# Optimization experiments

Hardware: AMD Instinct MI355X
Metric: run time of the kernel (lower is better)

The kernel has to match this reference:

```python
import jax, jax.numpy as jnp
import numpy as np

N = 10000
E = 320000
C = 16


def gcn_conv(x, edge_index, W, b, num_nodes):
    # PyG GCNConv: h = X W, then symmetric-normalized aggregation with self-loops, then + b
    h = x @ W  # [N, F_out]
    loop = jnp.arange(num_nodes, dtype=edge_index.dtype)
    src = jnp.concatenate([edge_index[0], loop])
    dst = jnp.concatenate([edge_index[1], loop])
    ones = jnp.ones(src.shape[0], dtype=h.dtype)
    deg = jax.ops.segment_sum(ones, dst, num_segments=num_nodes)  # in-degree incl. self-loop
    dinv = jnp.where(deg > 0, jax.lax.rsqrt(deg), 0.0)
    norm = dinv[src] * dinv[dst]  # [E+N]
    msg = h[src] * norm[:, None]  # gather + scale
    out = jax.ops.segment_sum(msg, dst, num_segments=num_nodes)  # scatter-add
    return out + b


def setup_inputs() -> dict:
    key = jax.random.key(0)
    ks = jax.random.split(key, 8)
    x = jax.random.normal(ks[0], (N, N), dtype=jnp.float32)
    edge_index = jax.random.randint(ks[1], (2, E), 0, N, dtype=jnp.int64)
    W1 = jax.random.normal(ks[2], (N, 64), dtype=jnp.float32) * (1.0 / np.sqrt(N))
    b1 = jnp.zeros((64,), dtype=jnp.float32)
    W2 = jax.random.normal(ks[3], (64, 64), dtype=jnp.float32) * (1.0 / 8.0)
    b2 = jnp.zeros((64,), dtype=jnp.float32)
    W3 = jax.random.normal(ks[4], (64, C), dtype=jnp.float32) * (1.0 / 8.0)
    b3 = jnp.zeros((C,), dtype=jnp.float32)
    return {"x": x, "edge_index": edge_index, "W1": W1, "b1": b1,
            "W2": W2, "b2": b2, "W3": W3, "b3": b3}


def reference(x, edge_index, W1, b1, W2, b2, W3, b3):
    h = jax.nn.relu(gcn_conv(x, edge_index, W1, b1, N))
    h = jax.nn.relu(gcn_conv(h, edge_index, W2, b2, N))
    h = gcn_conv(h, edge_index, W3, b3, N)
    return jax.nn.softmax(h, axis=1)
```

## Files before the change

kernel.cpp:

```cpp
#include <hip/hip_runtime.h>

#define N_NODES 10000
#define E_EDGES 320000
#define KP 10016

typedef float f32x4 __attribute__((ext_vector_type(4)));
typedef __bf16 bf16x8 __attribute__((ext_vector_type(8)));

union frag_u { int4 i; bf16x8 b; };

static __device__ __forceinline__ ushort f2bf(float f) {
    unsigned u = __float_as_uint(f);
    unsigned r = (u + 0x7fffu + ((u >> 16) & 1u)) >> 16;
    return (ushort)r;
}
static __device__ __forceinline__ float bf2f(ushort h) {
    return __uint_as_float(((unsigned)h) << 16);
}

static __device__ __forceinline__ void split2(float f0, float f1,
                                              unsigned& hi, unsigned& lo) {
    unsigned u0 = __float_as_uint(f0), u1 = __float_as_uint(f1);
    hi = __builtin_amdgcn_perm(u1, u0, 0x07060302u);
    float h0 = __uint_as_float(u0 & 0xFFFF0000u);
    float h1 = __uint_as_float(u1 & 0xFFFF0000u);
    float l0 = f0 - h0, l1 = f1 - h1;
    lo = __builtin_amdgcn_perm(__float_as_uint(l1), __float_as_uint(l0), 0x07060302u);
}

static __device__ __forceinline__ void load16_to_lds(const float* gp, void* lp) {
    __builtin_amdgcn_global_load_lds(
        (__attribute__((address_space(1))) void*)(gp),
        (__attribute__((address_space(3))) void*)(lp), 16, 0, 0);
}


#define HIST_BLOCKS (E_EDGES / 256)
#define WSPLIT_KB   ((KP + 255) / 256)
#define WSPLIT_BLOCKS (WSPLIT_KB * 64)

__global__ void k_hist_wsplit(const int* __restrict__ dst, int* __restrict__ deg,
                              const float* __restrict__ W1, ushort* __restrict__ Whi,
                              ushort* __restrict__ Wlo) {
    int bid = blockIdx.x;
    int tid = threadIdx.x;
    if (bid < HIST_BLOCKS) {
        int e = bid * 256 + tid;
        atomicAdd(&deg[dst[e]], 1);
    } else {
        int q = bid - HIST_BLOCKS;
        int n = q / WSPLIT_KB;
        int kb = q % WSPLIT_KB;
        int k = kb * 256 + tid;
        if (k >= KP) return;
        ushort h = 0, l = 0;
        if (k < N_NODES) {
            float f = W1[(long)k * 64 + n];
            h = f2bf(f);
            l = f2bf(f - bf2f(h));
        }
        Whi[(long)n * KP + k] = h;
        Wlo[(long)n * KP + k] = l;
    }
}


__global__ void k_scan(const int* __restrict__ deg, int* __restrict__ roff,
                       float* __restrict__ dinv) {
    __shared__ int sums[256];
    __shared__ int offs[256];
    const int CH = 40;
    int t = threadIdx.x;
    int base = t * CH;
    int s = 0;
    for (int i = 0; i < CH; i++) {
        int idx = base + i;
        if (idx < N_NODES) {
            int d = deg[idx];
            s += d;
            dinv[idx] = rsqrtf(1.0f + (float)d);
        }
    }
    sums[t] = s;
    __syncthreads();
    if (t == 0) {
        int r = 0;
        for (int i = 0; i < 256; i++) { offs[i] = r; r += sums[i]; }
    }
    __syncthreads();
    int r = offs[t];
    for (int i = 0; i < CH; i++) {
        int idx = base + i;
        if (idx < N_NODES) { roff[idx] = r; r += deg[idx]; }
    }
    if (t == 255) roff[N_NODES] = E_EDGES;
}

__global__ void k_scatter(const int* __restrict__ src, const int* __restrict__ dst,
                          const int* __restrict__ roff, int* __restrict__ cursor,
                          const float* __restrict__ dinv,
                          int* __restrict__ csrc, float* __restrict__ cw) {
    int e = blockIdx.x * blockDim.x + threadIdx.x;
    if (e >= E_EDGES) return;
    int s = src[e], d = dst[e];
    int slot = roff[d] + atomicAdd(&cursor[d], 1);
    csrc[slot] = s;
    cw[slot] = dinv[s] * dinv[d];
}


#define G1_BM 128
#define G1_CHUNK 640
#define G1_NCHUNK 16

__global__ __launch_bounds__(256) void k_gemm1_mfma(
        const float* __restrict__ x, const ushort* __restrict__ Whi,
        const ushort* __restrict__ Wlo, float* __restrict__ outP) {
    __shared__ float As32[2][G1_BM][32];
    __shared__ ushort Bs[2][2][64][40];

    int tid = threadIdx.x;
    int lane = tid & 63, wv = tid >> 6;
    int quad = lane >> 4, lm = lane & 15;
    int m0 = blockIdx.x * G1_BM;
    int ks = blockIdx.y * G1_CHUNK;
    int ke = min(ks + G1_CHUNK, KP);

    int rown = lane >> 3;
    int sp = (lane & 7) ^ rown;
    long abase[4];
#pragma unroll
    for (int i = 0; i < 4; i++) {
        int row = (wv * 4 + i) * 8 + rown;
        int gm = min(m0 + row, N_NODES - 1);
        abase[i] = (long)gm * N_NODES + sp * 4;
    }
    const long FLAT_MAX = (long)N_NODES * N_NODES - 4;

    int bn = tid >> 2, bp = (tid & 3) * 8;
    const ushort* whip = Whi + (long)bn * KP + bp;
    const ushort* wlop = Wlo + (long)bn * KP + bp;

    f32x4 acc[2][4] = {};

#pragma unroll
    for (int i = 0; i < 4; i++) {
        long flat = abase[i] + ks;
        if (flat > FLAT_MAX) flat = FLAT_MAX;
        load16_to_lds(x + flat, &As32[0][(wv * 4 + i) * 8][0]);
    }
    {
        float4 vh = *(const float4*)(whip + ks);
        float4 vl = *(const float4*)(wlop + ks);
        *(float4*)&Bs[0][0][bn][bp] = vh;
        *(float4*)&Bs[0][1][bn][bp] = vl;
    }
    __syncthreads();

    int cur = 0;
    for (int k0 = ks; k0 < ke; k0 += 32) {
        int kn = k0 + 32;
        bool pf = (kn < ke);
        float4 vh, vl;
        if (pf) {
#pragma unroll
            for (int i = 0; i < 4; i++) {
                long flat = abase[i] + kn;
                if (flat > FLAT_MAX) flat = FLAT_MAX;
                load16_to_lds(x + flat, &As32[cur ^ 1][(wv * 4 + i) * 8][0]);
            }
            vh = *(const float4*)(whip + kn);
            vl = *(const float4*)(wlop + kn);
        }

        frag_u ah[2], al[2];
#pragma unroll
        for (int r = 0; r < 2; r++) {
            int row = wv * 32 + r * 16 + lm;
            int r7 = row & 7;
            int s0 = (quad * 2) ^ r7;
            int s1 = (quad * 2 + 1) ^ r7;
            float4 fa = *(const float4*)&As32[cur][row][s0 * 4];
            float4 fb = *(const float4*)&As32[cur][row][s1 * 4];
            unsigned h0, l0, h1, l1, h2, l2, h3, l3;
            split2(fa.x, fa.y, h0, l0);
            split2(fa.z, fa.w, h1, l1);
            split2(fb.x, fb.y, h2, l2);
            split2(fb.z, fb.w, h3, l3);
            ah[r].i = make_int4((int)h0, (int)h1, (int)h2, (int)h3);
            al[r].i = make_int4((int)l0, (int)l1, (int)l2, (int)l3);
        }
        frag_u bh[4], bl[4];
#pragma unroll
        for (int c = 0; c < 4; c++) {
            int n = c * 16 + lm;
            bh[c].b = *(const bf16x8*)&Bs[cur][0][n][quad * 8];
            bl[c].b = *(const bf16x8*)&Bs[cur][1][n][quad * 8];
        }
#pragma unroll
        for (int r = 0; r < 2; r++)
#pragma unroll
            for (int c = 0; c < 4; c++) {
                acc[r][c] = __builtin_amdgcn_mfma_f32_16x16x32_bf16(al[r].b, bh[c].b, acc[r][c], 0, 0, 0);
                acc[r][c] = __builtin_amdgcn_mfma_f32_16x16x32_bf16(ah[r].b, bl[c].b, acc[r][c], 0, 0, 0);
                acc[r][c] = __builtin_amdgcn_mfma_f32_16x16x32_bf16(ah[r].b, bh[c].b, acc[r][c], 0, 0, 0);
            }

        if (pf) {
            asm volatile("s_waitcnt vmcnt(0)" ::: "memory");
            *(float4*)&Bs[cur ^ 1][0][bn][bp] = vh;
            *(float4*)&Bs[cur ^ 1][1][bn][bp] = vl;
        }
        asm volatile("s_waitcnt vmcnt(0) lgkmcnt(0)" ::: "memory");
        __builtin_amdgcn_s_barrier();
        cur ^= 1;
    }

    float* op = outP + (long)blockIdx.y * ((long)N_NODES * 64);
#pragma unroll
    for (int r = 0; r < 2; r++)
#pragma unroll
        for (int c = 0; c < 4; c++) {
            int row0 = m0 + wv * 32 + r * 16 + quad * 4;
            int cn = c * 16 + lm;
#pragma unroll
            for (int i = 0; i < 4; i++) {
                int gm = row0 + i;
                if (gm < N_NODES) op[(long)gm * 64 + cn] = acc[r][c][i];
            }
        }
}

__global__ void k_reduce16(const float* __restrict__ P, float* __restrict__ o) {
    int i = blockIdx.x * 256 + threadIdx.x;
    float s = 0.f;
#pragma unroll
    for (int j = 0; j < G1_NCHUNK; j++)
        s += P[(long)j * (N_NODES * 64) + i];
    o[i] = s;
}


__global__ void k_agg64(const float* __restrict__ h, const float* __restrict__ bias,
                        const int* __restrict__ roff, const int* __restrict__ csrc,
                        const float* __restrict__ cw, const float* __restrict__ dinv,
                        float* __restrict__ out, int do_relu) {
    int n = blockIdx.x * 4 + (threadIdx.x >> 6);
    int c = threadIdx.x & 63;
    float di = dinv[n];
    float acc = di * di * h[n * 64 + c];
    int e0 = roff[n], e1 = roff[n + 1];
    int e = e0;
    for (; e + 3 < e1; e += 4) {
        int s0 = csrc[e], s1 = csrc[e + 1], s2 = csrc[e + 2], s3 = csrc[e + 3];
        float w0 = cw[e], w1 = cw[e + 1], w2 = cw[e + 2], w3 = cw[e + 3];
        float v0 = h[s0 * 64 + c], v1 = h[s1 * 64 + c];
        float v2 = h[s2 * 64 + c], v3 = h[s3 * 64 + c];
        acc = fmaf(w0, v0, acc);
        acc = fmaf(w1, v1, acc);
        acc = fmaf(w2, v2, acc);
        acc = fmaf(w3, v3, acc);
    }
    for (; e < e1; e++)
        acc = fmaf(cw[e], h[csrc[e] * 64 + c], acc);
    acc += bias[c];
    if (do_relu) acc = fmaxf(acc, 0.f);
    out[n * 64 + c] = acc;
}


__global__ __launch_bounds__(256) void k_layer2(
        const float* __restrict__ h, const float* __restrict__ W2,
        const float* __restrict__ b2,
        const int* __restrict__ roff, const int* __restrict__ csrc,
        const float* __restrict__ cw, const float* __restrict__ dinv,
        float* __restrict__ out) {
    __shared__ float Ws[64 * 64];
    __shared__ float rowbuf[4][64];
    int tid = threadIdx.x;
    int w = tid >> 6, c = tid & 63;
    for (int f = tid; f < 1024; f += 256)
        *(float4*)&Ws[f * 4] = *(const float4*)&W2[f * 4];

    int n = blockIdx.x * 4 + w;
    float di = dinv[n];
    float acc = di * di * h[n * 64 + c];
    int e0 = roff[n], e1 = roff[n + 1];
    int e = e0;
    for (; e + 3 < e1; e += 4) {
        int s0 = csrc[e], s1 = csrc[e + 1], s2 = csrc[e + 2], s3 = csrc[e + 3];
        float w0 = cw[e], w1 = cw[e + 1], w2 = cw[e + 2], w3 = cw[e + 3];
        float v0 = h[s0 * 64 + c], v1 = h[s1 * 64 + c];
        float v2 = h[s2 * 64 + c], v3 = h[s3 * 64 + c];
        acc = fmaf(w0, v0, acc);
        acc = fmaf(w1, v1, acc);
        acc = fmaf(w2, v2, acc);
        acc = fmaf(w3, v3, acc);
    }
    for (; e < e1; e++)
        acc = fmaf(cw[e], h[csrc[e] * 64 + c], acc);
    rowbuf[w][c] = acc;
    __syncthreads();

    float o = b2[c];
#pragma unroll
    for (int k = 0; k < 64; k++)
        o = fmaf(rowbuf[w][k], Ws[k * 64 + c], o);
    o = fmaxf(o, 0.f);
    out[n * 64 + c] = o;
}


__global__ __launch_bounds__(256) void k_layer3(
        const float* __restrict__ h, const float* __restrict__ W3,
        const float* __restrict__ b3,
        const int* __restrict__ roff, const int* __restrict__ csrc,
        const float* __restrict__ cw, const float* __restrict__ dinv,
        float* __restrict__ out) {
    __shared__ float Ws[64 * 17];
    __shared__ float rowbuf[4][64];
    int tid = threadIdx.x;
    int w = tid >> 6, c = tid & 63;
    for (int f = tid; f < 1024; f += 256) {
        int kk = f >> 4, cc0 = f & 15;
        Ws[kk * 17 + cc0] = W3[f];
    }

    int n = blockIdx.x * 4 + w;
    float di = dinv[n];
    float acc = di * di * h[n * 64 + c];
    int e0 = roff[n], e1 = roff[n + 1];
    int e = e0;
    for (; e + 3 < e1; e += 4) {
        int s0 = csrc[e], s1 = csrc[e + 1], s2 = csrc[e + 2], s3 = csrc[e + 3];
        float w0 = cw[e], w1 = cw[e + 1], w2 = cw[e + 2], w3 = cw[e + 3];
        float v0 = h[s0 * 64 + c], v1 = h[s1 * 64 + c];
        float v2 = h[s2 * 64 + c], v3 = h[s3 * 64 + c];
        acc = fmaf(w0, v0, acc);
        acc = fmaf(w1, v1, acc);
        acc = fmaf(w2, v2, acc);
        acc = fmaf(w3, v3, acc);
    }
    for (; e < e1; e++)
        acc = fmaf(cw[e], h[csrc[e] * 16 + c & 0 ? 0 : csrc[e] * 64 + c], acc);
    rowbuf[w][c] = acc;
    __syncthreads();

    int cc = c & 15, g = c >> 4;
    float o = 0.f;
#pragma unroll
    for (int i = 0; i < 16; i++) {
        int k = g * 16 + i;
        o = fmaf(rowbuf[w][k], Ws[k * 17 + cc], o);
    }
    o += __shfl_xor(o, 16);
    o += __shfl_xor(o, 32);
    float logit = o + b3[cc];
    float m = logit;
    m = fmaxf(m, __shfl_xor(m, 1));
    m = fmaxf(m, __shfl_xor(m, 2));
    m = fmaxf(m, __shfl_xor(m, 4));
    m = fmaxf(m, __shfl_xor(m, 8));
    float ex = expf(logit - m);
    float s = ex;
    s += __shfl_xor(s, 1);
    s += __shfl_xor(s, 2);
    s += __shfl_xor(s, 4);
    s += __shfl_xor(s, 8);
    if (g == 0) out[n * 16 + cc] = ex / s;
}


extern "C" void kernel_launch(void* const* d_in, const int* in_sizes, int n_in,
                              void* d_out, int out_size, void* d_ws, size_t ws_size,
                              hipStream_t stream) {
    (void)in_sizes; (void)n_in; (void)out_size; (void)ws_size;
    const float* x  = (const float*)d_in[0];
    const int*   ei = (const int*)d_in[1];
    const float* W1 = (const float*)d_in[2];
    const float* b1 = (const float*)d_in[3];
    const float* W2 = (const float*)d_in[4];
    const float* b2 = (const float*)d_in[5];
    const float* W3 = (const float*)d_in[6];
    const float* b3 = (const float*)d_in[7];
    float* out = (float*)d_out;
    const int* esrc = ei;
    const int* edst = ei + E_EDGES;

    char* p = (char*)d_ws;
    size_t off = 0;
    auto alloc = [&](size_t b) -> void* {
        void* r = p + off;
        off += (b + 255) & ~(size_t)255;
        return r;
    };
    int*    deg    = (int*)alloc(N_NODES * 4);
    int*    cursor = (int*)alloc(N_NODES * 4);
    int*    roff   = (int*)alloc((N_NODES + 1) * 4);
    float*  dinv   = (float*)alloc(N_NODES * 4);
    int*    csrc   = (int*)alloc(E_EDGES * 4);
    float*  cw     = (float*)alloc(E_EDGES * 4);
    float*  bufA   = (float*)alloc((size_t)N_NODES * 64 * 4);
    float*  bufB   = (float*)alloc((size_t)N_NODES * 64 * 4);
    ushort* Whi    = (ushort*)alloc((size_t)64 * KP * 2);
    ushort* Wlo    = (ushort*)alloc((size_t)64 * KP * 2);
    float*  bufP   = (float*)alloc((size_t)G1_NCHUNK * N_NODES * 64 * 4);

    size_t zlen = (size_t)((char*)(cursor + N_NODES) - (char*)deg);
    hipMemsetAsync(deg, 0, zlen, stream);

    k_hist_wsplit<<<HIST_BLOCKS + WSPLIT_BLOCKS, 256, 0, stream>>>(edst, deg, W1, Whi, Wlo);
    k_scan<<<1, 256, 0, stream>>>(deg, roff, dinv);
    k_scatter<<<(E_EDGES + 255) / 256, 256, 0, stream>>>(esrc, edst, roff, cursor, dinv,
                                                         csrc, cw);

    k_gemm1_mfma<<<dim3((N_NODES + G1_BM - 1) / G1_BM, G1_NCHUNK), 256, 0, stream>>>(
        x, Whi, Wlo, bufP);
    k_reduce16<<<(N_NODES * 64) / 256, 256, 0, stream>>>(bufP, bufA);
    k_agg64<<<N_NODES / 4, 256, 0, stream>>>(bufA, b1, roff, csrc, cw, dinv, bufB, 1);
    k_layer2<<<N_NODES / 4, 256, 0, stream>>>(bufB, W2, b2, roff, csrc, cw, dinv, bufA);
    k_layer3<<<N_NODES / 4, 256, 0, stream>>>(bufA, W3, b3, roff, csrc, cw, dinv, out);
}
```

Measured before the change: 695.9 us.

## Load GEMM1 A operand directly to registers and reduce split-K with atomics

The first-layer GEMM no longer stages the fp32 x tile through LDS via global_load_lds. Each lane now loads its fragment directly from global memory into registers, and the wait on vector memory before the barrier is dropped. The split-K partial buffer and the separate reduce kernel are replaced by float atomicAdd into a zero-initialised output, with the memset range extended to cover it. This removes a large partial-sum write/read and one launch, but it gives up the LDS-based prefetch overlap for x, and the atomics make the summation order nondeterministic.

```diff
diff --git a/kernel.cpp b/kernel.cpp
--- a/kernel.cpp
+++ b/kernel.cpp
@@ -26,12 +26,6 @@
     float h1 = __uint_as_float(u1 & 0xFFFF0000u);
     float l0 = f0 - h0, l1 = f1 - h1;
     lo = __builtin_amdgcn_perm(__float_as_uint(l1), __float_as_uint(l0), 0x07060302u);
-}
-
-static __device__ __forceinline__ void load16_to_lds(const float* gp, void* lp) {
-    __builtin_amdgcn_global_load_lds(
-        (__attribute__((address_space(1))) void*)(gp),
-        (__attribute__((address_space(3))) void*)(lp), 16, 0, 0);
 }
 
 
@@ -115,8 +109,7 @@
 
 __global__ __launch_bounds__(256) void k_gemm1_mfma(
         const float* __restrict__ x, const ushort* __restrict__ Whi,
-        const ushort* __restrict__ Wlo, float* __restrict__ outP) {
-    __shared__ float As32[2][G1_BM][32];
+        const ushort* __restrict__ Wlo, float* __restrict__ out) {
     __shared__ ushort Bs[2][2][64][40];
 
     int tid = threadIdx.x;
@@ -126,16 +119,14 @@
     int ks = blockIdx.y * G1_CHUNK;
     int ke = min(ks + G1_CHUNK, KP);
 
-    int rown = lane >> 3;
-    int sp = (lane & 7) ^ rown;
-    long abase[4];
-#pragma unroll
-    for (int i = 0; i < 4; i++) {
-        int row = (wv * 4 + i) * 8 + rown;
-        int gm = min(m0 + row, N_NODES - 1);
-        abase[i] = (long)gm * N_NODES + sp * 4;
-    }
-    const long FLAT_MAX = (long)N_NODES * N_NODES - 4;
+    long arow[2];
+#pragma unroll
+    for (int r = 0; r < 2; r++) {
+        int row = m0 + wv * 32 + r * 16 + lm;
+        if (row > N_NODES - 1) row = N_NODES - 1;
+        arow[r] = (long)row * N_NODES + quad * 8;
+    }
+    const long FLAT_MAX = (long)N_NODES * N_NODES - 8;
 
     int bn = tid >> 2, bp = (tid & 3) * 8;
     const ushort* whip = Whi + (long)bn * KP + bp;
@@ -143,12 +134,6 @@
 
     f32x4 acc[2][4] = {};
 
-#pragma unroll
-    for (int i = 0; i < 4; i++) {
-        long flat = abase[i] + ks;
-        if (flat > FLAT_MAX) flat = FLAT_MAX;
-        load16_to_lds(x + flat, &As32[0][(wv * 4 + i) * 8][0]);
-    }
     {
         float4 vh = *(const float4*)(whip + ks);
         float4 vl = *(const float4*)(wlop + ks);
@@ -161,35 +146,21 @@
     for (int k0 = ks; k0 < ke; k0 += 32) {
         int kn = k0 + 32;
         bool pf = (kn < ke);
+
+        float4 fa[2], fb[2];
+#pragma unroll
+        for (int r = 0; r < 2; r++) {
+            long flat = arow[r] + k0;
+            if (flat > FLAT_MAX) flat = FLAT_MAX;
+            fa[r] = *(const float4*)(x + flat);
+            fb[r] = *(const float4*)(x + flat + 4);
+        }
         float4 vh, vl;
         if (pf) {
-#pragma unroll
-            for (int i = 0; i < 4; i++) {
-                long flat = abase[i] + kn;
-                if (flat > FLAT_MAX) flat = FLAT_MAX;
-                load16_to_lds(x + flat, &As32[cur ^ 1][(wv * 4 + i) * 8][0]);
-            }
             vh = *(const float4*)(whip + kn);
             vl = *(const float4*)(wlop + kn);
         }
 
-        frag_u ah[2], al[2];
-#pragma unroll
-        for (int r = 0; r < 2; r++) {
-            int row = wv * 32 + r * 16 + lm;
-            int r7 = row & 7;
-            int s0 = (quad * 2) ^ r7;
-            int s1 = (quad * 2 + 1) ^ r7;
-            float4 fa = *(const float4*)&As32[cur][row][s0 * 4];
-            float4 fb = *(const float4*)&As32[cur][row][s1 * 4];
-            unsigned h0, l0, h1, l1, h2, l2, h3, l3;
-            split2(fa.x, fa.y, h0, l0);
-            split2(fa.z, fa.w, h1, l1);
-            split2(fb.x, fb.y, h2, l2);
-            split2(fb.z, fb.w, h3, l3);
-            ah[r].i = make_int4((int)h0, (int)h1, (int)h2, (int)h3);
-            al[r].i = make_int4((int)l0, (int)l1, (int)l2, (int)l3);
-        }
         frag_u bh[4], bl[4];
 #pragma unroll
         for (int c = 0; c < 4; c++) {
@@ -197,6 +168,19 @@
             bh[c].b = *(const bf16x8*)&Bs[cur][0][n][quad * 8];
             bl[c].b = *(const bf16x8*)&Bs[cur][1][n][quad * 8];
         }
+
+        frag_u ah[2], al[2];
+#pragma unroll
+        for (int r = 0; r < 2; r++) {
+            unsigned h0, l0, h1, l1, h2, l2, h3, l3;
+            split2(fa[r].x, fa[r].y, h0, l0);
+            split2(fa[r].z, fa[r].w, h1, l1);
+            split2(fb[r].x, fb[r].y, h2, l2);
+            split2(fb[r].z, fb[r].w, h3, l3);
+            ah[r].i = make_int4((int)h0, (int)h1, (int)h2, (int)h3);
+            al[r].i = make_int4((int)l0, (int)l1, (int)l2, (int)l3);
+        }
+
 #pragma unroll
         for (int r = 0; r < 2; r++)
 #pragma unroll
@@ -211,12 +195,11 @@
             *(float4*)&Bs[cur ^ 1][0][bn][bp] = vh;
             *(float4*)&Bs[cur ^ 1][1][bn][bp] = vl;
         }
-        asm volatile("s_waitcnt vmcnt(0) lgkmcnt(0)" ::: "memory");
+        asm volatile("s_waitcnt lgkmcnt(0)" ::: "memory");
         __builtin_amdgcn_s_barrier();
         cur ^= 1;
     }
 
-    float* op = outP + (long)blockIdx.y * ((long)N_NODES * 64);
 #pragma unroll
     for (int r = 0; r < 2; r++)
 #pragma unroll
@@ -226,18 +209,9 @@
 #pragma unroll
             for (int i = 0; i < 4; i++) {
                 int gm = row0 + i;
-                if (gm < N_NODES) op[(long)gm * 64 + cn] = acc[r][c][i];
+                if (gm < N_NODES) atomicAdd(&out[gm * 64 + cn], acc[r][c][i]);
             }
         }
-}
-
-__global__ void k_reduce16(const float* __restrict__ P, float* __restrict__ o) {
-    int i = blockIdx.x * 256 + threadIdx.x;
-    float s = 0.f;
-#pragma unroll
-    for (int j = 0; j < G1_NCHUNK; j++)
-        s += P[(long)j * (N_NODES * 64) + i];
-    o[i] = s;
 }
 
 
@@ -342,7 +316,7 @@
         acc = fmaf(w3, v3, acc);
     }
     for (; e < e1; e++)
-        acc = fmaf(cw[e], h[csrc[e] * 16 + c & 0 ? 0 : csrc[e] * 64 + c], acc);
+        acc = fmaf(cw[e], h[csrc[e] * 64 + c], acc);
     rowbuf[w][c] = acc;
     __syncthreads();
 
@@ -396,17 +370,16 @@
     };
     int*    deg    = (int*)alloc(N_NODES * 4);
     int*    cursor = (int*)alloc(N_NODES * 4);
+    float*  bufA   = (float*)alloc((size_t)N_NODES * 64 * 4);
     int*    roff   = (int*)alloc((N_NODES + 1) * 4);
     float*  dinv   = (float*)alloc(N_NODES * 4);
     int*    csrc   = (int*)alloc(E_EDGES * 4);
     float*  cw     = (float*)alloc(E_EDGES * 4);
-    float*  bufA   = (float*)alloc((size_t)N_NODES * 64 * 4);
     float*  bufB   = (float*)alloc((size_t)N_NODES * 64 * 4);
     ushort* Whi    = (ushort*)alloc((size_t)64 * KP * 2);
     ushort* Wlo    = (ushort*)alloc((size_t)64 * KP * 2);
-    float*  bufP   = (float*)alloc((size_t)G1_NCHUNK * N_NODES * 64 * 4);
-
-    size_t zlen = (size_t)((char*)(cursor + N_NODES) - (char*)deg);
+
+    size_t zlen = (size_t)((char*)(bufA + (size_t)N_NODES * 64) - (char*)deg);
     hipMemsetAsync(deg, 0, zlen, stream);
 
     k_hist_wsplit<<<HIST_BLOCKS + WSPLIT_BLOCKS, 256, 0, stream>>>(edst, deg, W1, Whi, Wlo);
@@ -415,8 +388,7 @@
                                                          csrc, cw);
 
     k_gemm1_mfma<<<dim3((N_NODES + G1_BM - 1) / G1_BM, G1_NCHUNK), 256, 0, stream>>>(
-        x, Whi, Wlo, bufP);
-    k_reduce16<<<(N_NODES * 64) / 256, 256, 0, stream>>>(bufP, bufA);
+        x, Whi, Wlo, bufA);
     k_agg64<<<N_NODES / 4, 256, 0, stream>>>(bufA, b1, roff, csrc, cw, dinv, bufB, 1);
     k_layer2<<<N_NODES / 4, 256, 0, stream>>>(bufB, W2, b2, roff, csrc, cw, dinv, bufA);
     k_layer3<<<N_NODES / 4, 256, 0, stream>>>(bufA, W3, b3, roff, csrc, cw, dinv, out);
```

Measured after the change: 700.4 us. About the same (+0.6%).
